# Kernel optimization log

Hardware: AMD Instinct MI355X
Metric: run time of the kernel (lower is better)

The kernel has to match this reference:

```python
import jax, jax.numpy as jnp
import numpy as np

N = 100000
E = 500000
HID = 256
N_EDGE_TYPES = 5
N_ATOM = 16
N_CHARGE = 7
NUM_RBF = 16
CUTOFF = 5.0
LN_EPS = 1e-5


def _xavier(key, shape):
    fan_in, fan_out = shape[0], shape[1]
    lim = float(np.sqrt(6.0 / (fan_in + fan_out)))
    return jax.random.uniform(key, shape, jnp.float32, -lim, lim)


def setup_inputs() -> dict:
    key = jax.random.key(0)
    ks = jax.random.split(key, 12)
    input_dim = HID * 2 + NUM_RBF + N_ATOM + N_CHARGE  # 551
    h = jax.random.normal(ks[0], (N, HID), jnp.float32)
    x = jax.random.normal(ks[1], (N, 3), jnp.float32)
    spawn_node_idx = jax.random.randint(ks[2], (E,), 0, N)
    existing_node_idx = jax.random.randint(ks[3], (E,), 0, N)
    ins_x = jax.random.normal(ks[4], (E, 3), jnp.float32)
    ins_a = jax.random.randint(ks[5], (E,), 0, N_ATOM)
    ins_c = jax.random.randint(ks[6], (E,), 0, N_CHARGE)
    # MLP params (Xavier weights, zero biases; LayerNorm gamma=1, beta=0)
    W1 = _xavier(ks[7], (input_dim, HID)); b1 = jnp.zeros((HID,), jnp.float32)
    g1 = jnp.ones((HID,), jnp.float32); be1 = jnp.zeros((HID,), jnp.float32)
    W2 = _xavier(ks[8], (HID, HID // 2)); b2 = jnp.zeros((HID // 2,), jnp.float32)
    g2 = jnp.ones((HID // 2,), jnp.float32); be2 = jnp.zeros((HID // 2,), jnp.float32)
    W3 = _xavier(ks[9], (HID // 2, N_EDGE_TYPES)); b3 = jnp.zeros((N_EDGE_TYPES,), jnp.float32)
    # Gaussian RBF parameters: centers on [0, cutoff], shared width from spacing
    rbf_mu = jnp.linspace(0.0, CUTOFF, NUM_RBF).astype(jnp.float32)
    delta = CUTOFF / (NUM_RBF - 1)
    rbf_gamma = jnp.asarray(1.0 / (2.0 * delta * delta), jnp.float32)
    return {"h": h, "x": x, "spawn_node_idx": spawn_node_idx,
            "existing_node_idx": existing_node_idx, "ins_x": ins_x,
            "ins_a": ins_a, "ins_c": ins_c,
            "W1": W1, "b1": b1, "g1": g1, "be1": be1,
            "W2": W2, "b2": b2, "g2": g2, "be2": be2,
            "W3": W3, "b3": b3, "rbf_mu": rbf_mu, "rbf_gamma": rbf_gamma}


def _layer_norm(z, gamma, beta):
    mu = jnp.mean(z, axis=-1, keepdims=True)
    var = jnp.mean((z - mu) ** 2, axis=-1, keepdims=True)
    return (z - mu) * jax.lax.rsqrt(var + LN_EPS) * gamma + beta


def reference(h, x, spawn_node_idx, existing_node_idx, ins_x, ins_a, ins_c,
              W1, b1, g1, be1, W2, b2, g2, be2, W3, b3, rbf_mu, rbf_gamma):
    # gather node pairs  [E, HID] / [E, 3]
    h_spawn = h[spawn_node_idx]
    h_existing = h[existing_node_idx]
    existing_pos = x[existing_node_idx]
    # distance + Gaussian RBF  [E, NUM_RBF]
    d = jnp.maximum(jnp.linalg.norm(ins_x - existing_pos, axis=-1), 1e-6)
    dist_features = jnp.exp(-rbf_gamma * (d[:, None] - rbf_mu) ** 2)
    # one-hot insertion type features
    ins_atom = jax.nn.one_hot(ins_a, N_ATOM, dtype=h.dtype)
    ins_charge = jax.nn.one_hot(ins_c, N_CHARGE, dtype=h.dtype)
    feats = jnp.concatenate([h_spawn, h_existing, dist_features, ins_atom, ins_charge], axis=-1)
    # 3-layer MLP: Linear -> LN -> SiLU -> Linear -> LN -> SiLU -> Linear
    z = jax.nn.silu(_layer_norm(feats @ W1 + b1, g1, be1))
    z = jax.nn.silu(_layer_norm(z @ W2 + b2, g2, be2))
    return z @ W3 + b3  # [E, N_EDGE_TYPES]
```

## Files before the change

kernel.cpp:

```cpp
#include <hip/hip_runtime.h>
#include <stdint.h>

#define NN 100000
#define EE 500000
#define HIDD 256
#define LN_EPS 1e-5f

typedef _Float16 half8 __attribute__((ext_vector_type(8)));
typedef _Float16 half4 __attribute__((ext_vector_type(4)));
typedef __fp16 fp16x2 __attribute__((ext_vector_type(2)));
typedef float f32x4 __attribute__((ext_vector_type(4)));
typedef float f32x2 __attribute__((ext_vector_type(2)));

#define LBAR() asm volatile("s_waitcnt lgkmcnt(0)\n\ts_barrier" ::: "memory")

__device__ __forceinline__ unsigned short f2h(float f) {
  _Float16 h = (_Float16)f;
  union { _Float16 hh; unsigned short us; } u; u.hh = h;
  return u.us;
}

__device__ __forceinline__ unsigned pkrtz(float a, float b) {
  union { fp16x2 h; unsigned u; } c;
  c.h = __builtin_amdgcn_cvt_pkrtz(a, b);
  return c.u;
}

__device__ __forceinline__ float fast_silu(float y) {
  float e = __expf(-y);
  return y * __builtin_amdgcn_rcpf(1.f + e);
}

__device__ __forceinline__ half8 ldg8(const unsigned short* p) {
  return *(const half8*)p;
}

__device__ __forceinline__ int4 cvt_row(const float* s) {
  float4 a0 = *(const float4*)s, a1 = *(const float4*)(s + 4);
  uint4 ua;
  ua.x = pkrtz(a0.x, a0.y); ua.y = pkrtz(a0.z, a0.w);
  ua.z = pkrtz(a1.x, a1.y); ua.w = pkrtz(a1.z, a1.w);
  return *(int4*)&ua;
}

__global__ __launch_bounds__(256) void prep_kern(const float* __restrict__ h,
                                                 const float* __restrict__ W1,
                                                 const float* __restrict__ W2,
                                                 const float* __restrict__ W3,
                                                 unsigned short* __restrict__ hb,
                                                 unsigned short* __restrict__ w1sw,
                                                 unsigned short* __restrict__ w2sw,
                                                 unsigned short* __restrict__ w3sw) {
  int b = blockIdx.x;
  if (b < 712) {
    int t = b * 256 + threadIdx.x;
    if (t < 147456) {
      int chunk = t >> 14, rem = t & 16383;
      int kq = rem >> 11, n = (rem >> 3) & 255, j = rem & 7;
      int k = (chunk << 6) + (kq << 3) + j;
      float v = (k < 551) ? W1[k * 256 + n] : 0.f;
      w1sw[t] = f2h(v);
    } else if (t < 147456 + 32768) {
      int t2 = t - 147456;
      int chunk = t2 >> 13, rem = t2 & 8191;
      int kq = rem >> 10, n = (rem >> 3) & 127, j = rem & 7;
      int k = (chunk << 6) + (kq << 3) + j;
      w2sw[t2] = f2h(W2[k * 128 + n]);
    } else if (t < 147456 + 32768 + 2048) {
      int t3 = t - 180224;
      int kq = t3 >> 7, o = (t3 >> 3) & 15, j = t3 & 7;
      int k = (kq << 3) + j;
      w3sw[t3] = f2h((o < 5) ? W3[k * 5 + o] : 0.f);
    }
  } else {
    int i = ((b - 712) * 256 + threadIdx.x) * 8;
    float4 v0 = *(const float4*)(h + i);
    float4 v1 = *(const float4*)(h + i + 4);
    uint4 u;
    u.x = pkrtz(v0.x, v0.y); u.y = pkrtz(v0.z, v0.w);
    u.z = pkrtz(v1.x, v1.y); u.w = pkrtz(v1.z, v1.w);
    *(uint4*)(hb + i) = u;
  }
}

struct __align__(16) SMem {
  short r1[16384];
  short feats[4096];
  float red[512];
  _Float16 b1h[256], g1h[256], be1h[256];
  _Float16 b2h[128], g2h[128], be2h[128];
  float muv[16];
  float b3v[8];
  int spI[64], exI[64];
};

__global__ __launch_bounds__(256, 3)
void edge_head_main(const float* __restrict__ h, const float* __restrict__ x,
                    const int* __restrict__ spawn, const int* __restrict__ exist,
                    const float* __restrict__ insx, const int* __restrict__ insa,
                    const int* __restrict__ insc,
                    const float* __restrict__ b1, const float* __restrict__ g1,
                    const float* __restrict__ be1,
                    const float* __restrict__ b2, const float* __restrict__ g2,
                    const float* __restrict__ be2,
                    const float* __restrict__ b3, const float* __restrict__ mu,
                    const float* __restrict__ gammaP,
                    const unsigned short* __restrict__ w1sw,
                    const unsigned short* __restrict__ w2sw,
                    const unsigned short* __restrict__ w3swg,
                    const unsigned short* __restrict__ hb, int use_hb,
                    float* __restrict__ out) {
  __shared__ SMem sm;
  const int t = threadIdx.x;
  const int base = blockIdx.x * 64;
  const int lane = t & 63;
  const int wv = t >> 6;
  const int cl = lane & 15;
  const int q = lane >> 4;
  const int sx = (cl & 7) << 3;

  sm.b1h[t] = (_Float16)b1[t]; sm.g1h[t] = (_Float16)g1[t]; sm.be1h[t] = (_Float16)be1[t];
  if (t < 128) { sm.b2h[t] = (_Float16)b2[t]; sm.g2h[t] = (_Float16)g2[t]; sm.be2h[t] = (_Float16)be2[t]; }
  if (t < 16) sm.muv[t] = mu[t];
  if (t < 8) sm.b3v[t] = (t < 5) ? b3[t] : 0.f;
  if (t < 64) {
    int e = base + t; int ec = e < EE ? e : EE - 1;
    sm.spI[t] = spawn[ec]; sm.exI[t] = exist[ec];
  }
  const float gma = gammaP[0];

  LBAR();

  float dreg = 0.f;
  int k1 = 16, k2 = 32;
  if (t < 64) {
    int e = base + t; int ec = e < EE ? e : EE - 1;
    float ix0 = insx[ec * 3], ix1 = insx[ec * 3 + 1], ix2 = insx[ec * 3 + 2];
    int nd = sm.exI[t];
    float dx = ix0 - x[nd * 3], dy = ix1 - x[nd * 3 + 1], dz = ix2 - x[nd * 3 + 2];
    dreg = fmaxf(sqrtf(dx * dx + dy * dy + dz * dz), 1e-6f);
    k1 = 16 + insa[ec]; k2 = 32 + insc[ec];
  }

  const int row0 = t >> 3, p0 = t & 7;
  const int row1 = row0 + 32;
  const int sw0 = ((p0 ^ (row0 & 7)) << 3);
  const int sw1 = ((p0 ^ (row1 & 7)) << 3);

  const size_t oSp0 = (size_t)sm.spI[row0] * HIDD + p0 * 8;
  const size_t oSp1 = (size_t)sm.spI[row1] * HIDD + p0 * 8;
  const size_t oEx0 = (size_t)sm.exI[row0] * HIDD + p0 * 8;
  const size_t oEx1 = (size_t)sm.exI[row1] * HIDD + p0 * 8;
  const char* bSp0 = use_hb ? (const char*)(hb + oSp0) : (const char*)(h + oSp0);
  const char* bSp1 = use_hb ? (const char*)(hb + oSp1) : (const char*)(h + oSp1);
  const char* bEx0 = use_hb ? (const char*)(hb + oEx0) : (const char*)(h + oEx0);
  const char* bEx1 = use_hb ? (const char*)(hb + oEx1) : (const char*)(h + oEx1);

  int4 pS0, pS1, pS2, pS3;
#define GLOAD2(ph) do {                                                 \
    const char* b0_ = ((ph) < 2) ? bSp0 : bEx0;                         \
    const char* b1_ = ((ph) < 2) ? bSp1 : bEx1;                         \
    const int ce_ = ((ph) & 1) * 128;             \
    if (use_hb) {                                                       \
      pS0 = *(const int4*)(b0_ + ce_ * 2);                              \
      pS1 = *(const int4*)(b1_ + ce_ * 2);                              \
      pS2 = *(const int4*)(b0_ + (ce_ + 64) * 2);                       \
      pS3 = *(const int4*)(b1_ + (ce_ + 64) * 2);                       \
    } else {                                                            \
      pS0 = cvt_row((const float*)(b0_ + ce_ * 4));                     \
      pS1 = cvt_row((const float*)(b1_ + ce_ * 4));                     \
      pS2 = cvt_row((const float*)(b0_ + (ce_ + 64) * 4));              \
      pS3 = cvt_row((const float*)(b1_ + (ce_ + 64) * 4));              \
    }                                                                   \
  } while (0)

  GLOAD2(0);
  *(int4*)&sm.r1[row0 * 64 + sw0] = pS0;
  *(int4*)&sm.r1[row1 * 64 + sw1] = pS1;
  *(int4*)&sm.r1[4096 + row0 * 64 + sw0] = pS2;
  *(int4*)&sm.r1[4096 + row1 * 64 + sw1] = pS3;
  GLOAD2(1);

  const unsigned short* w1p = w1sw + q * 2048 + wv * 512 + cl * 8;

  if (t < 64) {
    short* rp = &sm.feats[t * 64];
    const int sw = t & 7;
    float rb[16];
#pragma unroll
    for (int k = 0; k < 16; ++k) { float dd = dreg - sm.muv[k]; rb[k] = __expf(-gma * dd * dd); }
    uint4 ua, ub;
    ua.x = pkrtz(rb[0], rb[1]);  ua.y = pkrtz(rb[2], rb[3]);
    ua.z = pkrtz(rb[4], rb[5]);  ua.w = pkrtz(rb[6], rb[7]);
    ub.x = pkrtz(rb[8], rb[9]);  ub.y = pkrtz(rb[10], rb[11]);
    ub.z = pkrtz(rb[12], rb[13]); ub.w = pkrtz(rb[14], rb[15]);
    *(int4*)&rp[(0 ^ sw) * 8] = *(int4*)&ua;
    *(int4*)&rp[(1 ^ sw) * 8] = *(int4*)&ub;
    const int4 z4 = {0, 0, 0, 0};
#pragma unroll
    for (int g = 2; g < 8; ++g) *(int4*)&rp[(g ^ sw) * 8] = z4;
    rp[((k1 >> 3) ^ sw) * 8 + (k1 & 7)] = (short)0x3C00;
    rp[((k2 >> 3) ^ sw) * 8 + (k2 & 7)] = (short)0x3C00;
  }

  LBAR();

  f32x4 acc[4][4];
#pragma unroll
  for (int i = 0; i < 4; ++i)
#pragma unroll
    for (int j = 0; j < 4; ++j) acc[i][j] = (f32x4){0.f, 0.f, 0.f, 0.f};

#pragma unroll
  for (int p = 0; p < 4; ++p) {
    if (p < 3) {
      const int nb = ((p + 1) & 1) * 8192;
      *(int4*)&sm.r1[nb + row0 * 64 + sw0] = pS0;
      *(int4*)&sm.r1[nb + row1 * 64 + sw1] = pS1;
      *(int4*)&sm.r1[nb + 4096 + row0 * 64 + sw0] = pS2;
      *(int4*)&sm.r1[nb + 4096 + row1 * 64 + sw1] = pS3;
      if (p < 2) GLOAD2(p + 2);
    }
    const int cb = (p & 1) * 8192;
#pragma unroll
    for (int ch = 0; ch < 2; ++ch) {
      const unsigned short* wp = w1p + (2 * p + ch) * 16384;
#pragma unroll
      for (int ks = 0; ks < 2; ++ks) {
        half8 bf[4], fX[4];
#pragma unroll
        for (int j = 0; j < 4; ++j)
          bf[j] = *(const half8*)&sm.r1[cb + ch * 4096 + (j * 16 + cl) * 64 + ((ks * 32 + q * 8) ^ sx)];
#pragma unroll
        for (int i = 0; i < 4; ++i) fX[i] = ldg8(wp + ks * 8192 + i * 128);
#pragma unroll
        for (int i = 0; i < 4; ++i)
#pragma unroll
          for (int j = 0; j < 4; ++j)
            acc[i][j] = __builtin_amdgcn_mfma_f32_16x16x32_f16(fX[i], bf[j], acc[i][j], 0, 0, 0);
      }
    }
    if (p < 3) LBAR();
  }
#undef GLOAD2

  {
    const unsigned short* wp = w1p + 8 * 16384;
#pragma unroll
    for (int ks = 0; ks < 2; ++ks) {
      half8 bf[4], fX[4];
#pragma unroll
      for (int j = 0; j < 4; ++j)
        bf[j] = *(const half8*)&sm.feats[(j * 16 + cl) * 64 + ((ks * 32 + q * 8) ^ sx)];
#pragma unroll
      for (int i = 0; i < 4; ++i) fX[i] = ldg8(wp + ks * 8192 + i * 128);
#pragma unroll
      for (int i = 0; i < 4; ++i)
#pragma unroll
        for (int j = 0; j < 4; ++j)
          acc[i][j] = __builtin_amdgcn_mfma_f32_16x16x32_f16(fX[i], bf[j], acc[i][j], 0, 0, 0);
    }
  }

  f32x2 bb1[4][2];
#pragma unroll
  for (int i = 0; i < 4; ++i) {
    half4 b4 = *(const half4*)&sm.b1h[wv * 64 + i * 16 + q * 4];
    bb1[i][0] = (f32x2){(float)b4[0], (float)b4[1]};
    bb1[i][1] = (f32x2){(float)b4[2], (float)b4[3]};
  }
  float S1arr[4], Q1arr[4];
#pragma unroll
  for (int j = 0; j < 4; ++j) {
    f32x2 S2 = (f32x2){0.f, 0.f}, Q2 = (f32x2){0.f, 0.f};
#pragma unroll
    for (int i = 0; i < 4; ++i) {
      f32x2 v0 = (f32x2){acc[i][j][0], acc[i][j][1]} + bb1[i][0];
      f32x2 v1 = (f32x2){acc[i][j][2], acc[i][j][3]} + bb1[i][1];
      acc[i][j][0] = v0[0]; acc[i][j][1] = v0[1];
      acc[i][j][2] = v1[0]; acc[i][j][3] = v1[1];
      S2 += v0 + v1;
      Q2 += v0 * v0;
      Q2 += v1 * v1;
    }
    float S = S2[0] + S2[1], Q = Q2[0] + Q2[1];
    S += __shfl_xor(S, 16); S += __shfl_xor(S, 32);
    Q += __shfl_xor(Q, 16); Q += __shfl_xor(Q, 32);
    S1arr[j] = S; Q1arr[j] = Q;
  }
  if (q == 0) {
#pragma unroll
    for (int j = 0; j < 4; ++j) {
      sm.red[wv * 64 + j * 16 + cl] = S1arr[j];
      sm.red[256 + wv * 64 + j * 16 + cl] = Q1arr[j];
    }
  }
  LBAR();
  f32x2 rs1[4], mr1[4];
#pragma unroll
  for (int j = 0; j < 4; ++j) {
    int m = j * 16 + cl;
    float S = sm.red[m] + sm.red[64 + m] + sm.red[128 + m] + sm.red[192 + m];
    float Q = sm.red[256 + m] + sm.red[320 + m] + sm.red[384 + m] + sm.red[448 + m];
    float mn = S * (1.f / 256.f);
    float rs = rsqrtf(Q * (1.f / 256.f) - mn * mn + LN_EPS);
    rs1[j] = (f32x2){rs, rs};
    mr1[j] = (f32x2){-mn * rs, -mn * rs};
  }
#pragma unroll
  for (int i = 0; i < 4; ++i) {
    half4 g4 = *(const half4*)&sm.g1h[wv * 64 + i * 16 + q * 4];
    half4 e4 = *(const half4*)&sm.be1h[wv * 64 + i * 16 + q * 4];
    f32x2 gg0 = (f32x2){(float)g4[0], (float)g4[1]}, gg1 = (f32x2){(float)g4[2], (float)g4[3]};
    f32x2 ee0 = (f32x2){(float)e4[0], (float)e4[1]}, ee1 = (f32x2){(float)e4[2], (float)e4[3]};
#pragma unroll
    for (int j = 0; j < 4; ++j) {
      f32x2 v0 = (f32x2){acc[i][j][0], acc[i][j][1]};
      f32x2 v1 = (f32x2){acc[i][j][2], acc[i][j][3]};
      f32x2 t0 = v0 * rs1[j] + mr1[j];
      f32x2 t1 = v1 * rs1[j] + mr1[j];
      f32x2 y0 = t0 * gg0 + ee0;
      f32x2 y1 = t1 * gg1 + ee1;
      float s0 = fast_silu(y0[0]), s1 = fast_silu(y0[1]);
      float s2 = fast_silu(y1[0]), s3 = fast_silu(y1[1]);
      uint2 w; w.x = pkrtz(s0, s1); w.y = pkrtz(s2, s3);
      int m = j * 16 + cl;
      int k0 = wv * 64 + i * 16 + q * 4;
      *(uint2*)&sm.r1[m * 256 + (k0 ^ ((m & 7) << 3))] = w;
    }
  }
  LBAR();

  half8 af3[4];
#pragma unroll
  for (int ks = 0; ks < 4; ++ks)
    af3[ks] = ldg8(w3swg + (ks * 4 + q) * 128 + cl * 8);

  const unsigned short* w2p = w2sw + q * 1024 + wv * 256 + cl * 8;
  f32x4 acc2[2][4];
#pragma unroll
  for (int i = 0; i < 2; ++i)
#pragma unroll
    for (int j = 0; j < 4; ++j) acc2[i][j] = (f32x4){0.f, 0.f, 0.f, 0.f};
#pragma unroll
  for (int c2 = 0; c2 < 4; ++c2) {
#pragma unroll
    for (int ks = 0; ks < 2; ++ks) {
      half8 a0 = ldg8(w2p + c2 * 8192 + ks * 4096);
      half8 a1 = ldg8(w2p + c2 * 8192 + ks * 4096 + 128);
      half8 bf[4];
#pragma unroll
      for (int j = 0; j < 4; ++j)
        bf[j] = *(const half8*)&sm.r1[(j * 16 + cl) * 256 + ((c2 * 64 + ks * 32 + q * 8) ^ sx)];
#pragma unroll
      for (int j = 0; j < 4; ++j) {
        acc2[0][j] = __builtin_amdgcn_mfma_f32_16x16x32_f16(a0, bf[j], acc2[0][j], 0, 0, 0);
        acc2[1][j] = __builtin_amdgcn_mfma_f32_16x16x32_f16(a1, bf[j], acc2[1][j], 0, 0, 0);
      }
    }
  }

  f32x2 bb2[2][2];
#pragma unroll
  for (int i = 0; i < 2; ++i) {
    half4 b4 = *(const half4*)&sm.b2h[wv * 32 + i * 16 + q * 4];
    bb2[i][0] = (f32x2){(float)b4[0], (float)b4[1]};
    bb2[i][1] = (f32x2){(float)b4[2], (float)b4[3]};
  }
  float S2arr[4], Q2arr[4];
#pragma unroll
  for (int j = 0; j < 4; ++j) {
    f32x2 S2 = (f32x2){0.f, 0.f}, Q2 = (f32x2){0.f, 0.f};
#pragma unroll
    for (int i = 0; i < 2; ++i) {
      f32x2 v0 = (f32x2){acc2[i][j][0], acc2[i][j][1]} + bb2[i][0];
      f32x2 v1 = (f32x2){acc2[i][j][2], acc2[i][j][3]} + bb2[i][1];
      acc2[i][j][0] = v0[0]; acc2[i][j][1] = v0[1];
      acc2[i][j][2] = v1[0]; acc2[i][j][3] = v1[1];
      S2 += v0 + v1;
      Q2 += v0 * v0;
      Q2 += v1 * v1;
    }
    float S = S2[0] + S2[1], Q = Q2[0] + Q2[1];
    S += __shfl_xor(S, 16); S += __shfl_xor(S, 32);
    Q += __shfl_xor(Q, 16); Q += __shfl_xor(Q, 32);
    S2arr[j] = S; Q2arr[j] = Q;
  }
  if (q == 0) {
#pragma unroll
    for (int j = 0; j < 4; ++j) {
      sm.red[wv * 64 + j * 16 + cl] = S2arr[j];
      sm.red[256 + wv * 64 + j * 16 + cl] = Q2arr[j];
    }
  }
  LBAR();
  f32x2 rs2[4], mr2[4];
#pragma unroll
  for (int j = 0; j < 4; ++j) {
    int m = j * 16 + cl;
    float S = sm.red[m] + sm.red[64 + m] + sm.red[128 + m] + sm.red[192 + m];
    float Q = sm.red[256 + m] + sm.red[320 + m] + sm.red[384 + m] + sm.red[448 + m];
    float mn = S * (1.f / 128.f);
    float rs = rsqrtf(Q * (1.f / 128.f) - mn * mn + LN_EPS);
    rs2[j] = (f32x2){rs, rs};
    mr2[j] = (f32x2){-mn * rs, -mn * rs};
  }
#pragma unroll
  for (int i = 0; i < 2; ++i) {
    half4 g4 = *(const half4*)&sm.g2h[wv * 32 + i * 16 + q * 4];
    half4 e4 = *(const half4*)&sm.be2h[wv * 32 + i * 16 + q * 4];
    f32x2 gg0 = (f32x2){(float)g4[0], (float)g4[1]}, gg1 = (f32x2){(float)g4[2], (float)g4[3]};
    f32x2 ee0 = (f32x2){(float)e4[0], (float)e4[1]}, ee1 = (f32x2){(float)e4[2], (float)e4[3]};
#pragma unroll
    for (int j = 0; j < 4; ++j) {
      f32x2 v0 = (f32x2){acc2[i][j][0], acc2[i][j][1]};
      f32x2 v1 = (f32x2){acc2[i][j][2], acc2[i][j][3]};
      f32x2 t0 = v0 * rs2[j] + mr2[j];
      f32x2 t1 = v1 * rs2[j] + mr2[j];
      f32x2 y0 = t0 * gg0 + ee0;
      f32x2 y1 = t1 * gg1 + ee1;
      float s0 = fast_silu(y0[0]), s1 = fast_silu(y0[1]);
      float s2 = fast_silu(y1[0]), s3 = fast_silu(y1[1]);
      uint2 w; w.x = pkrtz(s0, s1); w.y = pkrtz(s2, s3);
      int m = j * 16 + cl;
      int k0 = wv * 32 + i * 16 + q * 4;
      *(uint2*)&sm.r1[m * 128 + (k0 ^ ((m & 7) << 3))] = w;
    }
  }
  LBAR();

  f32x4 a3 = (f32x4){0.f, 0.f, 0.f, 0.f};
  const int m3 = wv * 16 + cl;
  const int sx3 = (m3 & 7) << 3;
#pragma unroll
  for (int ks = 0; ks < 4; ++ks) {
    half8 bfv = *(const half8*)&sm.r1[m3 * 128 + ((ks * 32 + q * 8) ^ sx3)];
    a3 = __builtin_amdgcn_mfma_f32_16x16x32_f16(af3[ks], bfv, a3, 0, 0, 0);
  }
#pragma unroll
  for (int r = 0; r < 4; ++r) {
    int o = q * 4 + r;
    if (o < 5) sm.red[m3 * 5 + o] = a3[r] + sm.b3v[o];
  }
  LBAR();
  if (t < 80) {
    size_t g = (size_t)base * 5 + (size_t)t * 4;
    if (g + 4 <= (size_t)EE * 5) {
      *(float4*)(out + g) = *(const float4*)&sm.red[t * 4];
    } else {
#pragma unroll
      for (int u = 0; u < 4; ++u)
        if (g + u < (size_t)EE * 5) out[g + u] = sm.red[t * 4 + u];
    }
  }
}

extern "C" void kernel_launch(void* const* d_in, const int* in_sizes, int n_in,
                              void* d_out, int out_size, void* d_ws, size_t ws_size,
                              hipStream_t stream) {
  const float* h    = (const float*)d_in[0];
  const float* x    = (const float*)d_in[1];
  const int* spawn  = (const int*)d_in[2];
  const int* exist  = (const int*)d_in[3];
  const float* insx = (const float*)d_in[4];
  const int* insa   = (const int*)d_in[5];
  const int* insc   = (const int*)d_in[6];
  const float* W1   = (const float*)d_in[7];
  const float* b1   = (const float*)d_in[8];
  const float* g1   = (const float*)d_in[9];
  const float* be1  = (const float*)d_in[10];
  const float* W2   = (const float*)d_in[11];
  const float* b2   = (const float*)d_in[12];
  const float* g2   = (const float*)d_in[13];
  const float* be2  = (const float*)d_in[14];
  const float* W3   = (const float*)d_in[15];
  const float* b3   = (const float*)d_in[16];
  const float* mu   = (const float*)d_in[17];
  const float* gma  = (const float*)d_in[18];

  unsigned short* w1sw = (unsigned short*)d_ws;
  unsigned short* w2sw = w1sw + 147456;
  unsigned short* w3sw = w2sw + 32768;
  unsigned short* hb   = w3sw + 2048;
  const size_t need_hb = 364544ull + (size_t)NN * HIDD * 2ull;
  int use_hb = (ws_size >= need_hb) ? 1 : 0;

  prep_kern<<<use_hb ? 13212 : 712, 256, 0, stream>>>(h, W1, W2, W3, hb, w1sw, w2sw, w3sw);
  edge_head_main<<<7813, 256, 0, stream>>>(h, x, spawn, exist, insx, insa, insc,
                                           b1, g1, be1, b2, g2, be2, b3, mu, gma,
                                           w1sw, w2sw, w3sw, hb, use_hb,
                                           (float*)d_out);
}
```

Before: 421.8 us.

## Precompute per-node projections of h through W1 before gathering per edge

Splits the first linear layer so the h_spawn and h_existing contributions are computed once per node (100k nodes) by a new GEMM kernel into an fp16 buffer P, rather than once per edge (500k edges). The edge kernel then gathers two 256-wide projected rows per edge and runs only the small K=64 tail (RBF and one-hot features) through MFMA. This removes most of the layer-1 FLOPs and the per-edge gather of raw h. In exchange it adds a 100k x 512 fp16 intermediate that must be written and read back, and it rounds the partial sums to fp16 before the bias and LayerNorm. A fallback path keeps the old design for when the workspace is too small.

```diff
diff --git a/kernel.cpp b/kernel.cpp
--- a/kernel.cpp
+++ b/kernel.cpp
@@ -43,47 +43,108 @@
   return *(int4*)&ua;
 }
 
-__global__ __launch_bounds__(256) void prep_kern(const float* __restrict__ h,
-                                                 const float* __restrict__ W1,
-                                                 const float* __restrict__ W2,
-                                                 const float* __restrict__ W3,
-                                                 unsigned short* __restrict__ hb,
-                                                 unsigned short* __restrict__ w1sw,
-                                                 unsigned short* __restrict__ w2sw,
-                                                 unsigned short* __restrict__ w3sw) {
-  int b = blockIdx.x;
-  if (b < 712) {
-    int t = b * 256 + threadIdx.x;
-    if (t < 147456) {
-      int chunk = t >> 14, rem = t & 16383;
-      int kq = rem >> 11, n = (rem >> 3) & 255, j = rem & 7;
-      int k = (chunk << 6) + (kq << 3) + j;
-      float v = (k < 551) ? W1[k * 256 + n] : 0.f;
-      w1sw[t] = f2h(v);
-    } else if (t < 147456 + 32768) {
-      int t2 = t - 147456;
-      int chunk = t2 >> 13, rem = t2 & 8191;
-      int kq = rem >> 10, n = (rem >> 3) & 127, j = rem & 7;
-      int k = (chunk << 6) + (kq << 3) + j;
-      w2sw[t2] = f2h(W2[k * 128 + n]);
-    } else if (t < 147456 + 32768 + 2048) {
-      int t3 = t - 180224;
-      int kq = t3 >> 7, o = (t3 >> 3) & 15, j = t3 & 7;
-      int k = (kq << 3) + j;
-      w3sw[t3] = f2h((o < 5) ? W3[k * 5 + o] : 0.f);
-    }
-  } else {
-    int i = ((b - 712) * 256 + threadIdx.x) * 8;
-    float4 v0 = *(const float4*)(h + i);
-    float4 v1 = *(const float4*)(h + i + 4);
-    uint4 u;
-    u.x = pkrtz(v0.x, v0.y); u.y = pkrtz(v0.z, v0.w);
-    u.z = pkrtz(v1.x, v1.y); u.w = pkrtz(v1.z, v1.w);
-    *(uint4*)(hb + i) = u;
-  }
-}
-
-struct __align__(16) SMem {
+
+__global__ __launch_bounds__(256) void prep_w(const float* __restrict__ W1,
+                                              const float* __restrict__ W2,
+                                              const float* __restrict__ W3,
+                                              unsigned short* __restrict__ wc,
+                                              unsigned short* __restrict__ w1f,
+                                              unsigned short* __restrict__ w2sw,
+                                              unsigned short* __restrict__ w3sw) {
+  int t = blockIdx.x * 256 + threadIdx.x;
+  if (t < 131072) {
+    int kq = t >> 12, mm = (t >> 3) & 511, j = t & 7;
+    int k = kq * 8 + j;
+    int row = k + ((mm < 256) ? 0 : 256);
+    wc[t] = f2h(W1[row * 256 + (mm & 255)]);
+  } else if (t < 147456) {
+    int t2 = t - 131072;
+    int kq = t2 >> 11, m = (t2 >> 3) & 255, j = t2 & 7;
+    int k = 512 + kq * 8 + j;
+    w1f[t2] = f2h((k < 551) ? W1[k * 256 + m] : 0.f);
+  } else if (t < 180224) {
+    int t2 = t - 147456;
+    int chunk = t2 >> 13, rem = t2 & 8191;
+    int kq = rem >> 10, n = (rem >> 3) & 127, j = rem & 7;
+    int k = (chunk << 6) + (kq << 3) + j;
+    w2sw[t2] = f2h(W2[k * 128 + n]);
+  } else if (t < 182272) {
+    int t3 = t - 180224;
+    int kq = t3 >> 7, o = (t3 >> 3) & 15, j = t3 & 7;
+    int k = (kq << 3) + j;
+    w3sw[t3] = f2h((o < 5) ? W3[k * 5 + o] : 0.f);
+  }
+}
+
+__global__ __launch_bounds__(256) void pgemm(const float* __restrict__ h,
+                                             const unsigned short* __restrict__ wc,
+                                             unsigned short* __restrict__ Pb) {
+  __shared__ short hl[16384];
+  const int bid = blockIdx.x;
+  const int tile = bid >> 1, ch = bid & 1;
+  const int nb = tile * 64;
+  const int t = threadIdx.x;
+  const int lane = t & 63;
+  const int wv = t >> 6;
+  const int cl = lane & 15;
+  const int q = lane >> 4;
+  const int sx = (cl & 7) << 3;
+
+  const int row0 = t >> 3, p0 = t & 7;
+  const int row1 = row0 + 32;
+  const int n0 = (nb + row0 < NN) ? nb + row0 : NN - 1;
+  const int n1 = (nb + row1 < NN) ? nb + row1 : NN - 1;
+  const int sw0e = (row0 & 7) << 3;
+  const int sw1e = (row1 & 7) << 3;
+#pragma unroll
+  for (int c = 0; c < 4; ++c) {
+    int4 v0 = cvt_row(h + (size_t)n0 * 256 + c * 64 + p0 * 8);
+    int4 v1 = cvt_row(h + (size_t)n1 * 256 + c * 64 + p0 * 8);
+    *(int4*)&hl[row0 * 256 + ((c * 64 + p0 * 8) ^ sw0e)] = v0;
+    *(int4*)&hl[row1 * 256 + ((c * 64 + p0 * 8) ^ sw1e)] = v1;
+  }
+  LBAR();
+
+  const unsigned short* wcp = wc + q * 4096 + (size_t)(ch * 256 + wv * 64 + cl) * 8;
+  f32x4 acc[4][4];
+#pragma unroll
+  for (int i = 0; i < 4; ++i)
+#pragma unroll
+    for (int j = 0; j < 4; ++j) acc[i][j] = (f32x4){0.f, 0.f, 0.f, 0.f};
+
+#pragma unroll
+  for (int c = 0; c < 4; ++c)
+#pragma unroll
+    for (int ks = 0; ks < 2; ++ks) {
+      half8 bf[4], fX[4];
+#pragma unroll
+      for (int j = 0; j < 4; ++j)
+        bf[j] = *(const half8*)&hl[(j * 16 + cl) * 256 + ((c * 64 + ks * 32 + q * 8) ^ sx)];
+#pragma unroll
+      for (int i = 0; i < 4; ++i) fX[i] = ldg8(wcp + (c * 2 + ks) * 16384 + i * 128);
+#pragma unroll
+      for (int i = 0; i < 4; ++i)
+#pragma unroll
+        for (int j = 0; j < 4; ++j)
+          acc[i][j] = __builtin_amdgcn_mfma_f32_16x16x32_f16(fX[i], bf[j], acc[i][j], 0, 0, 0);
+    }
+
+#pragma unroll
+  for (int i = 0; i < 4; ++i)
+#pragma unroll
+    for (int j = 0; j < 4; ++j) {
+      int n = nb + cl + 16 * j;
+      if (n < NN) {
+        int mm = ch * 256 + wv * 64 + i * 16 + q * 4;
+        uint2 w;
+        w.x = pkrtz(acc[i][j][0], acc[i][j][1]);
+        w.y = pkrtz(acc[i][j][2], acc[i][j][3]);
+        *(uint2*)(Pb + (size_t)n * 512 + mm) = w;
+      }
+    }
+}
+
+struct __align__(16) SMemN {
   short r1[16384];
   short feats[4096];
   float red[512];
@@ -95,7 +156,7 @@
 };
 
 __global__ __launch_bounds__(256, 3)
-void edge_head_main(const float* __restrict__ h, const float* __restrict__ x,
+void edge_head_main(const float* __restrict__ x,
                     const int* __restrict__ spawn, const int* __restrict__ exist,
                     const float* __restrict__ insx, const int* __restrict__ insa,
                     const int* __restrict__ insc,
@@ -105,12 +166,12 @@
                     const float* __restrict__ be2,
                     const float* __restrict__ b3, const float* __restrict__ mu,
                     const float* __restrict__ gammaP,
-                    const unsigned short* __restrict__ w1sw,
+                    const unsigned short* __restrict__ w1f,
                     const unsigned short* __restrict__ w2sw,
                     const unsigned short* __restrict__ w3swg,
-                    const unsigned short* __restrict__ hb, int use_hb,
+                    const unsigned short* __restrict__ Pb,
                     float* __restrict__ out) {
-  __shared__ SMem sm;
+  __shared__ SMemN sm;
   const int t = threadIdx.x;
   const int base = blockIdx.x * 64;
   const int lane = t & 63;
@@ -131,64 +192,36 @@
 
   LBAR();
 
-  float dreg = 0.f;
-  int k1 = 16, k2 = 32;
+  const unsigned short* pb1[4];
+  const unsigned short* pb2[4];
+#pragma unroll
+  for (int j = 0; j < 4; ++j) {
+    int n = cl + 16 * j;
+    pb1[j] = Pb + (size_t)sm.spI[n] * 512 + wv * 64 + q * 4;
+    pb2[j] = Pb + (size_t)sm.exI[n] * 512 + 256 + wv * 64 + q * 4;
+  }
+  half4 p1v[4][4], p2v[4][4];
+#pragma unroll
+  for (int i = 0; i < 4; ++i)
+#pragma unroll
+    for (int j = 0; j < 4; ++j) p1v[i][j] = *(const half4*)(pb1[j] + i * 16);
+#pragma unroll
+  for (int i = 0; i < 4; ++i)
+#pragma unroll
+    for (int j = 0; j < 4; ++j) p2v[i][j] = *(const half4*)(pb2[j] + i * 16);
+
   if (t < 64) {
     int e = base + t; int ec = e < EE ? e : EE - 1;
     float ix0 = insx[ec * 3], ix1 = insx[ec * 3 + 1], ix2 = insx[ec * 3 + 2];
     int nd = sm.exI[t];
     float dx = ix0 - x[nd * 3], dy = ix1 - x[nd * 3 + 1], dz = ix2 - x[nd * 3 + 2];
-    dreg = fmaxf(sqrtf(dx * dx + dy * dy + dz * dz), 1e-6f);
-    k1 = 16 + insa[ec]; k2 = 32 + insc[ec];
-  }
-
-  const int row0 = t >> 3, p0 = t & 7;
-  const int row1 = row0 + 32;
-  const int sw0 = ((p0 ^ (row0 & 7)) << 3);
-  const int sw1 = ((p0 ^ (row1 & 7)) << 3);
-
-  const size_t oSp0 = (size_t)sm.spI[row0] * HIDD + p0 * 8;
-  const size_t oSp1 = (size_t)sm.spI[row1] * HIDD + p0 * 8;
-  const size_t oEx0 = (size_t)sm.exI[row0] * HIDD + p0 * 8;
-  const size_t oEx1 = (size_t)sm.exI[row1] * HIDD + p0 * 8;
-  const char* bSp0 = use_hb ? (const char*)(hb + oSp0) : (const char*)(h + oSp0);
-  const char* bSp1 = use_hb ? (const char*)(hb + oSp1) : (const char*)(h + oSp1);
-  const char* bEx0 = use_hb ? (const char*)(hb + oEx0) : (const char*)(h + oEx0);
-  const char* bEx1 = use_hb ? (const char*)(hb + oEx1) : (const char*)(h + oEx1);
-
-  int4 pS0, pS1, pS2, pS3;
-#define GLOAD2(ph) do {                                                 \
-    const char* b0_ = ((ph) < 2) ? bSp0 : bEx0;                         \
-    const char* b1_ = ((ph) < 2) ? bSp1 : bEx1;                         \
-    const int ce_ = ((ph) & 1) * 128;             \
-    if (use_hb) {                                                       \
-      pS0 = *(const int4*)(b0_ + ce_ * 2);                              \
-      pS1 = *(const int4*)(b1_ + ce_ * 2);                              \
-      pS2 = *(const int4*)(b0_ + (ce_ + 64) * 2);                       \
-      pS3 = *(const int4*)(b1_ + (ce_ + 64) * 2);                       \
-    } else {                                                            \
-      pS0 = cvt_row((const float*)(b0_ + ce_ * 4));                     \
-      pS1 = cvt_row((const float*)(b1_ + ce_ * 4));                     \
-      pS2 = cvt_row((const float*)(b0_ + (ce_ + 64) * 4));              \
-      pS3 = cvt_row((const float*)(b1_ + (ce_ + 64) * 4));              \
-    }                                                                   \
-  } while (0)
-
-  GLOAD2(0);
-  *(int4*)&sm.r1[row0 * 64 + sw0] = pS0;
-  *(int4*)&sm.r1[row1 * 64 + sw1] = pS1;
-  *(int4*)&sm.r1[4096 + row0 * 64 + sw0] = pS2;
-  *(int4*)&sm.r1[4096 + row1 * 64 + sw1] = pS3;
-  GLOAD2(1);
-
-  const unsigned short* w1p = w1sw + q * 2048 + wv * 512 + cl * 8;
-
-  if (t < 64) {
+    float d = fmaxf(sqrtf(dx * dx + dy * dy + dz * dz), 1e-6f);
+    int k1 = 16 + insa[ec], k2 = 32 + insc[ec];
     short* rp = &sm.feats[t * 64];
     const int sw = t & 7;
     float rb[16];
 #pragma unroll
-    for (int k = 0; k < 16; ++k) { float dd = dreg - sm.muv[k]; rb[k] = __expf(-gma * dd * dd); }
+    for (int k = 0; k < 16; ++k) { float dd = d - sm.muv[k]; rb[k] = __expf(-gma * dd * dd); }
     uint4 ua, ub;
     ua.x = pkrtz(rb[0], rb[1]);  ua.y = pkrtz(rb[2], rb[3]);
     ua.z = pkrtz(rb[4], rb[5]);  ua.w = pkrtz(rb[6], rb[7]);
@@ -209,43 +242,16 @@
 #pragma unroll
   for (int i = 0; i < 4; ++i)
 #pragma unroll
-    for (int j = 0; j < 4; ++j) acc[i][j] = (f32x4){0.f, 0.f, 0.f, 0.f};
-
-#pragma unroll
-  for (int p = 0; p < 4; ++p) {
-    if (p < 3) {
-      const int nb = ((p + 1) & 1) * 8192;
-      *(int4*)&sm.r1[nb + row0 * 64 + sw0] = pS0;
-      *(int4*)&sm.r1[nb + row1 * 64 + sw1] = pS1;
-      *(int4*)&sm.r1[nb + 4096 + row0 * 64 + sw0] = pS2;
-      *(int4*)&sm.r1[nb + 4096 + row1 * 64 + sw1] = pS3;
-      if (p < 2) GLOAD2(p + 2);
-    }
-    const int cb = (p & 1) * 8192;
-#pragma unroll
-    for (int ch = 0; ch < 2; ++ch) {
-      const unsigned short* wp = w1p + (2 * p + ch) * 16384;
-#pragma unroll
-      for (int ks = 0; ks < 2; ++ks) {
-        half8 bf[4], fX[4];
-#pragma unroll
-        for (int j = 0; j < 4; ++j)
-          bf[j] = *(const half8*)&sm.r1[cb + ch * 4096 + (j * 16 + cl) * 64 + ((ks * 32 + q * 8) ^ sx)];
-#pragma unroll
-        for (int i = 0; i < 4; ++i) fX[i] = ldg8(wp + ks * 8192 + i * 128);
-#pragma unroll
-        for (int i = 0; i < 4; ++i)
-#pragma unroll
-          for (int j = 0; j < 4; ++j)
-            acc[i][j] = __builtin_amdgcn_mfma_f32_16x16x32_f16(fX[i], bf[j], acc[i][j], 0, 0, 0);
-      }
-    }
-    if (p < 3) LBAR();
-  }
-#undef GLOAD2
-
+    for (int j = 0; j < 4; ++j) {
+      f32x4 a;
+      a[0] = (float)p1v[i][j][0] + (float)p2v[i][j][0];
+      a[1] = (float)p1v[i][j][1] + (float)p2v[i][j][1];
+      a[2] = (float)p1v[i][j][2] + (float)p2v[i][j][2];
+      a[3] = (float)p1v[i][j][3] + (float)p2v[i][j][3];
+      acc[i][j] = a;
+    }
   {
-    const unsigned short* wp = w1p + 8 * 16384;
+    const unsigned short* w1fp = w1f + q * 2048 + wv * 512 + cl * 8;
 #pragma unroll
     for (int ks = 0; ks < 2; ++ks) {
       half8 bf[4], fX[4];
@@ -253,7 +259,7 @@
       for (int j = 0; j < 4; ++j)
         bf[j] = *(const half8*)&sm.feats[(j * 16 + cl) * 64 + ((ks * 32 + q * 8) ^ sx)];
 #pragma unroll
-      for (int i = 0; i < 4; ++i) fX[i] = ldg8(wp + ks * 8192 + i * 128);
+      for (int i = 0; i < 4; ++i) fX[i] = ldg8(w1fp + ks * 8192 + i * 128);
 #pragma unroll
       for (int i = 0; i < 4; ++i)
 #pragma unroll
@@ -380,6 +386,387 @@
       S2 += v0 + v1;
       Q2 += v0 * v0;
       Q2 += v1 * v1;
+    }
+    float S = S2[0] + S2[1], Q = Q2[0] + Q2[1];
+    S += __shfl_xor(S, 16); S += __shfl_xor(S, 32);
+    Q += __shfl_xor(Q, 16); Q += __shfl_xor(Q, 32);
+    S2arr[j] = S; Q2arr[j] = Q;
+  }
+  if (q == 0) {
+#pragma unroll
+    for (int j = 0; j < 4; ++j) {
+      sm.red[wv * 64 + j * 16 + cl] = S2arr[j];
+      sm.red[256 + wv * 64 + j * 16 + cl] = Q2arr[j];
+    }
+  }
+  LBAR();
+  f32x2 rs2[4], mr2[4];
+#pragma unroll
+  for (int j = 0; j < 4; ++j) {
+    int m = j * 16 + cl;
+    float S = sm.red[m] + sm.red[64 + m] + sm.red[128 + m] + sm.red[192 + m];
+    float Q = sm.red[256 + m] + sm.red[320 + m] + sm.red[384 + m] + sm.red[448 + m];
+    float mn = S * (1.f / 128.f);
+    float rs = rsqrtf(Q * (1.f / 128.f) - mn * mn + LN_EPS);
+    rs2[j] = (f32x2){rs, rs};
+    mr2[j] = (f32x2){-mn * rs, -mn * rs};
+  }
+#pragma unroll
+  for (int i = 0; i < 2; ++i) {
+    half4 g4 = *(const half4*)&sm.g2h[wv * 32 + i * 16 + q * 4];
+    half4 e4 = *(const half4*)&sm.be2h[wv * 32 + i * 16 + q * 4];
+    f32x2 gg0 = (f32x2){(float)g4[0], (float)g4[1]}, gg1 = (f32x2){(float)g4[2], (float)g4[3]};
+    f32x2 ee0 = (f32x2){(float)e4[0], (float)e4[1]}, ee1 = (f32x2){(float)e4[2], (float)e4[3]};
+#pragma unroll
+    for (int j = 0; j < 4; ++j) {
+      f32x2 v0 = (f32x2){acc2[i][j][0], acc2[i][j][1]};
+      f32x2 v1 = (f32x2){acc2[i][j][2], acc2[i][j][3]};
+      f32x2 t0 = v0 * rs2[j] + mr2[j];
+      f32x2 t1 = v1 * rs2[j] + mr2[j];
+      f32x2 y0 = t0 * gg0 + ee0;
+      f32x2 y1 = t1 * gg1 + ee1;
+      float s0 = fast_silu(y0[0]), s1 = fast_silu(y0[1]);
+      float s2 = fast_silu(y1[0]), s3 = fast_silu(y1[1]);
+      uint2 w; w.x = pkrtz(s0, s1); w.y = pkrtz(s2, s3);
+      int m = j * 16 + cl;
+      int k0 = wv * 32 + i * 16 + q * 4;
+      *(uint2*)&sm.r1[m * 128 + (k0 ^ ((m & 7) << 3))] = w;
+    }
+  }
+  LBAR();
+
+  f32x4 a3 = (f32x4){0.f, 0.f, 0.f, 0.f};
+  const int m3 = wv * 16 + cl;
+  const int sx3 = (m3 & 7) << 3;
+#pragma unroll
+  for (int ks = 0; ks < 4; ++ks) {
+    half8 bfv = *(const half8*)&sm.r1[m3 * 128 + ((ks * 32 + q * 8) ^ sx3)];
+    a3 = __builtin_amdgcn_mfma_f32_16x16x32_f16(af3[ks], bfv, a3, 0, 0, 0);
+  }
+#pragma unroll
+  for (int r = 0; r < 4; ++r) {
+    int o = q * 4 + r;
+    if (o < 5) sm.red[m3 * 5 + o] = a3[r] + sm.b3v[o];
+  }
+  LBAR();
+  if (t < 80) {
+    size_t g = (size_t)base * 5 + (size_t)t * 4;
+    if (g + 4 <= (size_t)EE * 5) {
+      *(float4*)(out + g) = *(const float4*)&sm.red[t * 4];
+    } else {
+#pragma unroll
+      for (int u = 0; u < 4; ++u)
+        if (g + u < (size_t)EE * 5) out[g + u] = sm.red[t * 4 + u];
+    }
+  }
+}
+
+
+__global__ __launch_bounds__(256) void prep_fb(const float* __restrict__ W1,
+                                               const float* __restrict__ W2,
+                                               const float* __restrict__ W3,
+                                               unsigned short* __restrict__ w1sw,
+                                               unsigned short* __restrict__ w2sw,
+                                               unsigned short* __restrict__ w3sw) {
+  int t = blockIdx.x * 256 + threadIdx.x;
+  if (t < 147456) {
+    int chunk = t >> 14, rem = t & 16383;
+    int kq = rem >> 11, n = (rem >> 3) & 255, j = rem & 7;
+    int k = (chunk << 6) + (kq << 3) + j;
+    w1sw[t] = f2h((k < 551) ? W1[k * 256 + n] : 0.f);
+  } else if (t < 180224) {
+    int t2 = t - 147456;
+    int chunk = t2 >> 13, rem = t2 & 8191;
+    int kq = rem >> 10, n = (rem >> 3) & 127, j = rem & 7;
+    int k = (chunk << 6) + (kq << 3) + j;
+    w2sw[t2] = f2h(W2[k * 128 + n]);
+  } else if (t < 182272) {
+    int t3 = t - 180224;
+    int kq = t3 >> 7, o = (t3 >> 3) & 15, j = t3 & 7;
+    int k = (kq << 3) + j;
+    w3sw[t3] = f2h((o < 5) ? W3[k * 5 + o] : 0.f);
+  }
+}
+
+struct __align__(16) SMemF {
+  short r1[16384];
+  short feats[4096];
+  float red[512];
+  _Float16 b1h[256], g1h[256], be1h[256];
+  _Float16 b2h[128], g2h[128], be2h[128];
+  float muv[16];
+  float b3v[8];
+  int spI[64], exI[64];
+};
+
+__global__ __launch_bounds__(256, 3)
+void edge_head_fb(const float* __restrict__ h, const float* __restrict__ x,
+                  const int* __restrict__ spawn, const int* __restrict__ exist,
+                  const float* __restrict__ insx, const int* __restrict__ insa,
+                  const int* __restrict__ insc,
+                  const float* __restrict__ b1, const float* __restrict__ g1,
+                  const float* __restrict__ be1,
+                  const float* __restrict__ b2, const float* __restrict__ g2,
+                  const float* __restrict__ be2,
+                  const float* __restrict__ b3, const float* __restrict__ mu,
+                  const float* __restrict__ gammaP,
+                  const unsigned short* __restrict__ w1sw,
+                  const unsigned short* __restrict__ w2sw,
+                  const unsigned short* __restrict__ w3swg,
+                  float* __restrict__ out) {
+  __shared__ SMemF sm;
+  const int t = threadIdx.x;
+  const int base = blockIdx.x * 64;
+  const int lane = t & 63;
+  const int wv = t >> 6;
+  const int cl = lane & 15;
+  const int q = lane >> 4;
+  const int sx = (cl & 7) << 3;
+
+  sm.b1h[t] = (_Float16)b1[t]; sm.g1h[t] = (_Float16)g1[t]; sm.be1h[t] = (_Float16)be1[t];
+  if (t < 128) { sm.b2h[t] = (_Float16)b2[t]; sm.g2h[t] = (_Float16)g2[t]; sm.be2h[t] = (_Float16)be2[t]; }
+  if (t < 16) sm.muv[t] = mu[t];
+  if (t < 8) sm.b3v[t] = (t < 5) ? b3[t] : 0.f;
+  if (t < 64) {
+    int e = base + t; int ec = e < EE ? e : EE - 1;
+    sm.spI[t] = spawn[ec]; sm.exI[t] = exist[ec];
+  }
+  const float gma = gammaP[0];
+  LBAR();
+
+  float dreg = 0.f;
+  int k1 = 16, k2 = 32;
+  if (t < 64) {
+    int e = base + t; int ec = e < EE ? e : EE - 1;
+    float ix0 = insx[ec * 3], ix1 = insx[ec * 3 + 1], ix2 = insx[ec * 3 + 2];
+    int nd = sm.exI[t];
+    float dx = ix0 - x[nd * 3], dy = ix1 - x[nd * 3 + 1], dz = ix2 - x[nd * 3 + 2];
+    dreg = fmaxf(sqrtf(dx * dx + dy * dy + dz * dz), 1e-6f);
+    k1 = 16 + insa[ec]; k2 = 32 + insc[ec];
+  }
+
+  const int row0 = t >> 3, p0 = t & 7;
+  const int row1 = row0 + 32;
+  const int sw0 = ((p0 ^ (row0 & 7)) << 3);
+  const int sw1 = ((p0 ^ (row1 & 7)) << 3);
+
+  const float* bSp0 = h + (size_t)sm.spI[row0] * HIDD + p0 * 8;
+  const float* bSp1 = h + (size_t)sm.spI[row1] * HIDD + p0 * 8;
+  const float* bEx0 = h + (size_t)sm.exI[row0] * HIDD + p0 * 8;
+  const float* bEx1 = h + (size_t)sm.exI[row1] * HIDD + p0 * 8;
+
+  int4 pS0, pS1, pS2, pS3;
+#define GLOAD2F(ph) do {                                                \
+    const float* b0_ = ((ph) < 2) ? bSp0 : bEx0;                        \
+    const float* b1_ = ((ph) < 2) ? bSp1 : bEx1;                        \
+    const int ce_ = ((ph) & 1) * 128;                                   \
+    pS0 = cvt_row(b0_ + ce_);                                           \
+    pS1 = cvt_row(b1_ + ce_);                                           \
+    pS2 = cvt_row(b0_ + ce_ + 64);                                      \
+    pS3 = cvt_row(b1_ + ce_ + 64);                                      \
+  } while (0)
+
+  GLOAD2F(0);
+  *(int4*)&sm.r1[row0 * 64 + sw0] = pS0;
+  *(int4*)&sm.r1[row1 * 64 + sw1] = pS1;
+  *(int4*)&sm.r1[4096 + row0 * 64 + sw0] = pS2;
+  *(int4*)&sm.r1[4096 + row1 * 64 + sw1] = pS3;
+  GLOAD2F(1);
+
+  const unsigned short* w1p = w1sw + q * 2048 + wv * 512 + cl * 8;
+
+  if (t < 64) {
+    short* rp = &sm.feats[t * 64];
+    const int sw = t & 7;
+    float rb[16];
+#pragma unroll
+    for (int k = 0; k < 16; ++k) { float dd = dreg - sm.muv[k]; rb[k] = __expf(-gma * dd * dd); }
+    uint4 ua, ub;
+    ua.x = pkrtz(rb[0], rb[1]);  ua.y = pkrtz(rb[2], rb[3]);
+    ua.z = pkrtz(rb[4], rb[5]);  ua.w = pkrtz(rb[6], rb[7]);
+    ub.x = pkrtz(rb[8], rb[9]);  ub.y = pkrtz(rb[10], rb[11]);
+    ub.z = pkrtz(rb[12], rb[13]); ub.w = pkrtz(rb[14], rb[15]);
+    *(int4*)&rp[(0 ^ sw) * 8] = *(int4*)&ua;
+    *(int4*)&rp[(1 ^ sw) * 8] = *(int4*)&ub;
+    const int4 z4 = {0, 0, 0, 0};
+#pragma unroll
+    for (int g = 2; g < 8; ++g) *(int4*)&rp[(g ^ sw) * 8] = z4;
+    rp[((k1 >> 3) ^ sw) * 8 + (k1 & 7)] = (short)0x3C00;
+    rp[((k2 >> 3) ^ sw) * 8 + (k2 & 7)] = (short)0x3C00;
+  }
+  LBAR();
+
+  f32x4 acc[4][4];
+#pragma unroll
+  for (int i = 0; i < 4; ++i)
+#pragma unroll
+    for (int j = 0; j < 4; ++j) acc[i][j] = (f32x4){0.f, 0.f, 0.f, 0.f};
+
+#pragma unroll
+  for (int p = 0; p < 4; ++p) {
+    if (p < 3) {
+      const int nb = ((p + 1) & 1) * 8192;
+      *(int4*)&sm.r1[nb + row0 * 64 + sw0] = pS0;
+      *(int4*)&sm.r1[nb + row1 * 64 + sw1] = pS1;
+      *(int4*)&sm.r1[nb + 4096 + row0 * 64 + sw0] = pS2;
+      *(int4*)&sm.r1[nb + 4096 + row1 * 64 + sw1] = pS3;
+      if (p < 2) GLOAD2F(p + 2);
+    }
+    const int cb = (p & 1) * 8192;
+#pragma unroll
+    for (int ch = 0; ch < 2; ++ch) {
+      const unsigned short* wp = w1p + (2 * p + ch) * 16384;
+#pragma unroll
+      for (int ks = 0; ks < 2; ++ks) {
+        half8 bf[4], fX[4];
+#pragma unroll
+        for (int j = 0; j < 4; ++j)
+          bf[j] = *(const half8*)&sm.r1[cb + ch * 4096 + (j * 16 + cl) * 64 + ((ks * 32 + q * 8) ^ sx)];
+#pragma unroll
+        for (int i = 0; i < 4; ++i) fX[i] = ldg8(wp + ks * 8192 + i * 128);
+#pragma unroll
+        for (int i = 0; i < 4; ++i)
+#pragma unroll
+          for (int j = 0; j < 4; ++j)
+            acc[i][j] = __builtin_amdgcn_mfma_f32_16x16x32_f16(fX[i], bf[j], acc[i][j], 0, 0, 0);
+      }
+    }
+    if (p < 3) LBAR();
+  }
+#undef GLOAD2F
+
+  {
+    const unsigned short* wp = w1p + 8 * 16384;
+#pragma unroll
+    for (int ks = 0; ks < 2; ++ks) {
+      half8 bf[4], fX[4];
+#pragma unroll
+      for (int j = 0; j < 4; ++j)
+        bf[j] = *(const half8*)&sm.feats[(j * 16 + cl) * 64 + ((ks * 32 + q * 8) ^ sx)];
+#pragma unroll
+      for (int i = 0; i < 4; ++i) fX[i] = ldg8(wp + ks * 8192 + i * 128);
+#pragma unroll
+      for (int i = 0; i < 4; ++i)
+#pragma unroll
+        for (int j = 0; j < 4; ++j)
+          acc[i][j] = __builtin_amdgcn_mfma_f32_16x16x32_f16(fX[i], bf[j], acc[i][j], 0, 0, 0);
+    }
+  }
+
+  f32x2 bb1[4][2];
+#pragma unroll
+  for (int i = 0; i < 4; ++i) {
+    half4 b4 = *(const half4*)&sm.b1h[wv * 64 + i * 16 + q * 4];
+    bb1[i][0] = (f32x2){(float)b4[0], (float)b4[1]};
+    bb1[i][1] = (f32x2){(float)b4[2], (float)b4[3]};
+  }
+  float S1arr[4], Q1arr[4];
+#pragma unroll
+  for (int j = 0; j < 4; ++j) {
+    f32x2 S2 = (f32x2){0.f, 0.f}, Q2 = (f32x2){0.f, 0.f};
+#pragma unroll
+    for (int i = 0; i < 4; ++i) {
+      f32x2 v0 = (f32x2){acc[i][j][0], acc[i][j][1]} + bb1[i][0];
+      f32x2 v1 = (f32x2){acc[i][j][2], acc[i][j][3]} + bb1[i][1];
+      acc[i][j][0] = v0[0]; acc[i][j][1] = v0[1];
+      acc[i][j][2] = v1[0]; acc[i][j][3] = v1[1];
+      S2 += v0 + v1; Q2 += v0 * v0; Q2 += v1 * v1;
+    }
+    float S = S2[0] + S2[1], Q = Q2[0] + Q2[1];
+    S += __shfl_xor(S, 16); S += __shfl_xor(S, 32);
+    Q += __shfl_xor(Q, 16); Q += __shfl_xor(Q, 32);
+    S1arr[j] = S; Q1arr[j] = Q;
+  }
+  if (q == 0) {
+#pragma unroll
+    for (int j = 0; j < 4; ++j) {
+      sm.red[wv * 64 + j * 16 + cl] = S1arr[j];
+      sm.red[256 + wv * 64 + j * 16 + cl] = Q1arr[j];
+    }
+  }
+  LBAR();
+  f32x2 rs1[4], mr1[4];
+#pragma unroll
+  for (int j = 0; j < 4; ++j) {
+    int m = j * 16 + cl;
+    float S = sm.red[m] + sm.red[64 + m] + sm.red[128 + m] + sm.red[192 + m];
+    float Q = sm.red[256 + m] + sm.red[320 + m] + sm.red[384 + m] + sm.red[448 + m];
+    float mn = S * (1.f / 256.f);
+    float rs = rsqrtf(Q * (1.f / 256.f) - mn * mn + LN_EPS);
+    rs1[j] = (f32x2){rs, rs};
+    mr1[j] = (f32x2){-mn * rs, -mn * rs};
+  }
+#pragma unroll
+  for (int i = 0; i < 4; ++i) {
+    half4 g4 = *(const half4*)&sm.g1h[wv * 64 + i * 16 + q * 4];
+    half4 e4 = *(const half4*)&sm.be1h[wv * 64 + i * 16 + q * 4];
+    f32x2 gg0 = (f32x2){(float)g4[0], (float)g4[1]}, gg1 = (f32x2){(float)g4[2], (float)g4[3]};
+    f32x2 ee0 = (f32x2){(float)e4[0], (float)e4[1]}, ee1 = (f32x2){(float)e4[2], (float)e4[3]};
+#pragma unroll
+    for (int j = 0; j < 4; ++j) {
+      f32x2 v0 = (f32x2){acc[i][j][0], acc[i][j][1]};
+      f32x2 v1 = (f32x2){acc[i][j][2], acc[i][j][3]};
+      f32x2 t0 = v0 * rs1[j] + mr1[j];
+      f32x2 t1 = v1 * rs1[j] + mr1[j];
+      f32x2 y0 = t0 * gg0 + ee0;
+      f32x2 y1 = t1 * gg1 + ee1;
+      float s0 = fast_silu(y0[0]), s1 = fast_silu(y0[1]);
+      float s2 = fast_silu(y1[0]), s3 = fast_silu(y1[1]);
+      uint2 w; w.x = pkrtz(s0, s1); w.y = pkrtz(s2, s3);
+      int m = j * 16 + cl;
+      int k0 = wv * 64 + i * 16 + q * 4;
+      *(uint2*)&sm.r1[m * 256 + (k0 ^ ((m & 7) << 3))] = w;
+    }
+  }
+  LBAR();
+
+  half8 af3[4];
+#pragma unroll
+  for (int ks = 0; ks < 4; ++ks)
+    af3[ks] = ldg8(w3swg + (ks * 4 + q) * 128 + cl * 8);
+
+  const unsigned short* w2p = w2sw + q * 1024 + wv * 256 + cl * 8;
+  f32x4 acc2[2][4];
+#pragma unroll
+  for (int i = 0; i < 2; ++i)
+#pragma unroll
+    for (int j = 0; j < 4; ++j) acc2[i][j] = (f32x4){0.f, 0.f, 0.f, 0.f};
+#pragma unroll
+  for (int c2 = 0; c2 < 4; ++c2) {
+#pragma unroll
+    for (int ks = 0; ks < 2; ++ks) {
+      half8 a0 = ldg8(w2p + c2 * 8192 + ks * 4096);
+      half8 a1 = ldg8(w2p + c2 * 8192 + ks * 4096 + 128);
+      half8 bf[4];
+#pragma unroll
+      for (int j = 0; j < 4; ++j)
+        bf[j] = *(const half8*)&sm.r1[(j * 16 + cl) * 256 + ((c2 * 64 + ks * 32 + q * 8) ^ sx)];
+#pragma unroll
+      for (int j = 0; j < 4; ++j) {
+        acc2[0][j] = __builtin_amdgcn_mfma_f32_16x16x32_f16(a0, bf[j], acc2[0][j], 0, 0, 0);
+        acc2[1][j] = __builtin_amdgcn_mfma_f32_16x16x32_f16(a1, bf[j], acc2[1][j], 0, 0, 0);
+      }
+    }
+  }
+
+  f32x2 bb2[2][2];
+#pragma unroll
+  for (int i = 0; i < 2; ++i) {
+    half4 b4 = *(const half4*)&sm.b2h[wv * 32 + i * 16 + q * 4];
+    bb2[i][0] = (f32x2){(float)b4[0], (float)b4[1]};
+    bb2[i][1] = (f32x2){(float)b4[2], (float)b4[3]};
+  }
+  float S2arr[4], Q2arr[4];
+#pragma unroll
+  for (int j = 0; j < 4; ++j) {
+    f32x2 S2 = (f32x2){0.f, 0.f}, Q2 = (f32x2){0.f, 0.f};
+#pragma unroll
+    for (int i = 0; i < 2; ++i) {
+      f32x2 v0 = (f32x2){acc2[i][j][0], acc2[i][j][1]} + bb2[i][0];
+      f32x2 v1 = (f32x2){acc2[i][j][2], acc2[i][j][3]} + bb2[i][1];
+      acc2[i][j][0] = v0[0]; acc2[i][j][1] = v0[1];
+      acc2[i][j][2] = v1[0]; acc2[i][j][3] = v1[1];
+      S2 += v0 + v1; Q2 += v0 * v0; Q2 += v1 * v1;
     }
     float S = S2[0] + S2[1], Q = Q2[0] + Q2[1];
     S += __shfl_xor(S, 16); S += __shfl_xor(S, 32);
@@ -478,16 +865,25 @@
   const float* mu   = (const float*)d_in[17];
   const float* gma  = (const float*)d_in[18];
 
-  unsigned short* w1sw = (unsigned short*)d_ws;
-  unsigned short* w2sw = w1sw + 147456;
-  unsigned short* w3sw = w2sw + 32768;
-  unsigned short* hb   = w3sw + 2048;
-  const size_t need_hb = 364544ull + (size_t)NN * HIDD * 2ull;
-  int use_hb = (ws_size >= need_hb) ? 1 : 0;
-
-  prep_kern<<<use_hb ? 13212 : 712, 256, 0, stream>>>(h, W1, W2, W3, hb, w1sw, w2sw, w3sw);
-  edge_head_main<<<7813, 256, 0, stream>>>(h, x, spawn, exist, insx, insa, insc,
+  const size_t needP = 364544ull + (size_t)NN * 512 * 2;
+  if (ws_size >= needP) {
+    unsigned short* wc   = (unsigned short*)d_ws;
+    unsigned short* w1f  = wc + 131072;
+    unsigned short* w2sw = w1f + 16384;
+    unsigned short* w3sw = w2sw + 32768;
+    unsigned short* Pb   = w3sw + 2048;
+    prep_w<<<712, 256, 0, stream>>>(W1, W2, W3, wc, w1f, w2sw, w3sw);
+    pgemm<<<3126, 256, 0, stream>>>(h, wc, Pb);
+    edge_head_main<<<7813, 256, 0, stream>>>(x, spawn, exist, insx, insa, insc,
+                                             b1, g1, be1, b2, g2, be2, b3, mu, gma,
+                                             w1f, w2sw, w3sw, Pb, (float*)d_out);
+  } else {
+    unsigned short* w1sw = (unsigned short*)d_ws;
+    unsigned short* w2sw = w1sw + 147456;
+    unsigned short* w3sw = w2sw + 32768;
+    prep_fb<<<712, 256, 0, stream>>>(W1, W2, W3, w1sw, w2sw, w3sw);
+    edge_head_fb<<<7813, 256, 0, stream>>>(h, x, spawn, exist, insx, insa, insc,
                                            b1, g1, be1, b2, g2, be2, b3, mu, gma,
-                                           w1sw, w2sw, w3sw, hb, use_hb,
-                                           (float*)d_out);
-}
+                                           w1sw, w2sw, w3sw, (float*)d_out);
+  }
+}
```

After: 427.4 us. No clear change (+1.3%).
